# Kernel optimization log

Measured on AMD Instinct MI355X. Metric: run time of the kernel, lower is better.

Reference implementation:

```python
import jax, jax.numpy as jnp
import numpy as np

DIM = 512
HIDDEN = 2048
D_M = 256
R = 64
GEN_HIDDEN = D_M * 2  # hidden_mul=2
ALPHA_MEM = 1.0


def setup_inputs() -> dict:
    key = jax.random.key(0)
    ks = jax.random.split(key, 12)
    B, T = 2, 512
    inp = {
        'x': jax.random.normal(ks[0], (B, T, DIM), jnp.float32),
        'm_tok': jax.random.normal(ks[1], (B, T, D_M), jnp.float32),
        # base SwiGLU params
        'W1': jax.random.normal(ks[2], (HIDDEN, DIM), jnp.float32) * (1.0 / np.sqrt(DIM)),
        'W2': jax.random.normal(ks[3], (HIDDEN, DIM), jnp.float32) * (1.0 / np.sqrt(DIM)),
        'W3': jax.random.normal(ks[4], (DIM, HIDDEN), jnp.float32) * (1.0 / np.sqrt(HIDDEN)),
        'b1': jnp.zeros((HIDDEN,), jnp.float32),
        'b2': jnp.zeros((HIDDEN,), jnp.float32),
        'b3': jnp.zeros((DIM,), jnp.float32),
        # hypernetwork (FFNMemGenerator): d_m -> gen_hidden -> 3*r*dim
        'gen_w1': jax.random.normal(ks[5], (GEN_HIDDEN, D_M), jnp.float32) * (1.0 / np.sqrt(D_M)),
        'gen_b1': jnp.zeros((GEN_HIDDEN,), jnp.float32),
        'gen_w2': jax.random.normal(ks[6], (3 * R * DIM, GEN_HIDDEN), jnp.float32) * (0.02 / np.sqrt(GEN_HIDDEN)),
        'gen_b2': jnp.zeros((3 * R * DIM,), jnp.float32),
        'mem_gate': jnp.zeros((), jnp.float32),
    }
    return inp


def reference(x, m_tok, W1, W2, W3, b1, b2, b3, gen_w1, gen_b1, gen_w2, gen_b2, mem_gate):
    B, T, _ = x.shape
    # base SwiGLU FFN
    x1 = jnp.einsum('od,btd->bto', W1, x) + b1  # [B,T,hidden]
    x2 = jnp.einsum('od,btd->bto', W2, x) + b2
    h_base = jax.nn.silu(x1) * x2
    y_base = jnp.einsum('do,bto->btd', W3, h_base) + b3  # [B,T,dim]

    # hypernetwork-generated per-token low-rank weights
    hg = jax.nn.silu(jnp.einsum('hd,btd->bth', gen_w1, m_tok) + gen_b1)
    w = jnp.einsum('oh,bth->bto', gen_w2, hg) + gen_b2  # [B,T,3*r*dim]
    W1_m = w[..., : R * DIM].reshape(B, T, R, DIM)
    W2_m = w[..., R * DIM : 2 * R * DIM].reshape(B, T, R, DIM)
    W3_m = w[..., 2 * R * DIM :].reshape(B, T, DIM, R)

    # per-token batched matvecs (memory path)
    u1 = jnp.einsum('btrd,btd->btr', W1_m, x)
    u2 = jnp.einsum('btrd,btd->btr', W2_m, x)
    h_mem = jax.nn.silu(u1) * u2
    y_mem = jnp.einsum('btdr,btr->btd', W3_m, h_mem)

    g = jax.nn.sigmoid(mem_gate)
    return y_base + g * ALPHA_MEM * y_mem
```

## Files before the change

kernel.cpp:

```cpp
#include <hip/hip_runtime.h>
#include <cstdint>
#include <cstddef>

#define TOK   1024
#define DIMX  512
#define HID   2048
#define DM    256
#define GENH  512
#define RR    64
#define O3BASE 65536

typedef __bf16 bf16x8 __attribute__((ext_vector_type(8)));
typedef float  f32x4  __attribute__((ext_vector_type(4)));
typedef unsigned short u16x8 __attribute__((ext_vector_type(8)));

#define SB0 __builtin_amdgcn_sched_barrier(0)
#define BAR __builtin_amdgcn_s_barrier()

__device__ __forceinline__ unsigned short f2bf(float f) {
  union { float f; uint32_t u; } v; v.f = f;
  return (unsigned short)((v.u + 0x7fffu + ((v.u >> 16) & 1u)) >> 16);
}
__device__ __forceinline__ float bf2f(unsigned short h) {
  union { uint32_t u; float f; } v; v.u = (uint32_t)h << 16;
  return v.f;
}
__device__ __forceinline__ float silu_f(float x) { return x / (1.f + __expf(-x)); }

__device__ __forceinline__ u16x8 cvt8_hw(float4 a, float4 b) {
  union { __bf16 h; unsigned short u; } c;
  u16x8 r;
  c.h = (__bf16)a.x; r[0] = c.u; c.h = (__bf16)a.y; r[1] = c.u;
  c.h = (__bf16)a.z; r[2] = c.u; c.h = (__bf16)a.w; r[3] = c.u;
  c.h = (__bf16)b.x; r[4] = c.u; c.h = (__bf16)b.y; r[5] = c.u;
  c.h = (__bf16)b.z; r[6] = c.u; c.h = (__bf16)b.w; r[7] = c.u;
  return r;
}

__device__ __forceinline__ void async_copy16(const void* g, void* l) {
  __builtin_amdgcn_global_load_lds(
      (const __attribute__((address_space(1))) void*)g,
      (__attribute__((address_space(3))) void*)l, 16, 0, 0);
}

__device__ __forceinline__ float4 gldx4(const float* p) {
  float4 r;
  asm volatile("global_load_dwordx4 %0, %1, off" : "=v"(r) : "v"(p));
  return r;
}

__device__ __forceinline__ void cast8(const float* __restrict__ src,
                                      unsigned short* __restrict__ dst, size_t i) {
  float4 v0 = *(const float4*)(src + i);
  float4 v1 = *(const float4*)(src + i + 4);
  ushort4 h0, h1;
  h0.x = f2bf(v0.x); h0.y = f2bf(v0.y); h0.z = f2bf(v0.z); h0.w = f2bf(v0.w);
  h1.x = f2bf(v1.x); h1.y = f2bf(v1.y); h1.z = f2bf(v1.z); h1.w = f2bf(v1.w);
  *(ushort4*)(dst + i)     = h0;
  *(ushort4*)(dst + i + 4) = h1;
}

template<int ROWS>
__device__ __forceinline__ void stage_tile(
    const unsigned short* __restrict__ base, size_t row0, int stride, int kofs,
    unsigned short* Ls, int tid) {
  constexpr int IT = ROWS / 32;
  const int wave = tid >> 6, lane = tid & 63;
#pragma unroll
  for (int j = 0; j < IT; ++j) {
    int s   = wave * (IT * 64) + j * 64 + lane;
    int row = s >> 3;
    int kc  = (s & 7) ^ (row & 7);
    const unsigned short* g = base + (row0 + (size_t)row) * (size_t)stride + kofs + kc * 8;
    async_copy16(g, (char*)Ls + wave * (IT * 1024) + j * 1024);
  }
}

template<int KLEN, int MF>
__device__ __forceinline__ void mfma_tile_nt(
    const unsigned short* __restrict__ Abf, size_t a_row0, int astride,
    const unsigned short* __restrict__ Bbf, size_t b_row0, int bstride, int k0,
    unsigned short* As, unsigned short* Bs, f32x4 (&acc)[MF][4], int tid) {
  const int lane = tid & 63;
  const int wave = tid >> 6;
  const int m0 = (wave >> 1) * (MF * 16), n0 = (wave & 1) * 64;

  for (int kk = 0; kk < KLEN; kk += 64) {
    stage_tile<MF * 32>(Abf, a_row0, astride, k0 + kk, As, tid);
    stage_tile<128>(Bbf, b_row0, bstride, k0 + kk, Bs, tid);
    __syncthreads();
#pragma unroll
    for (int ks = 0; ks < 2; ++ks) {
      int cbase = ks * 4 + (lane >> 4);
      int koff  = (cbase ^ (lane & 7)) * 8;
      bf16x8 a[MF], b[4];
#pragma unroll
      for (int mf = 0; mf < MF; ++mf)
        a[mf] = *(const bf16x8*)(As + (m0 + mf * 16 + (lane & 15)) * 64 + koff);
#pragma unroll
      for (int nf = 0; nf < 4; ++nf)
        b[nf] = *(const bf16x8*)(Bs + (n0 + nf * 16 + (lane & 15)) * 64 + koff);
#pragma unroll
      for (int mf = 0; mf < MF; ++mf)
#pragma unroll
        for (int nf = 0; nf < 4; ++nf)
          acc[mf][nf] = __builtin_amdgcn_mfma_f32_16x16x32_bf16(
              a[mf], b[nf], acc[mf][nf], 0, 0, 0);
    }
    __syncthreads();
  }
}

template<int MF>
__device__ __forceinline__ void zero_accN(f32x4 (&acc)[MF][4]) {
#pragma unroll
  for (int i = 0; i < MF; ++i)
#pragma unroll
    for (int j = 0; j < 4; ++j) {
      f32x4 z = {0.f, 0.f, 0.f, 0.f};
      acc[i][j] = z;
    }
}

__device__ __forceinline__ void mfma_256_8ph(
    const unsigned short* __restrict__ Abf, size_t a_row0,
    const float* __restrict__ Bf, size_t b_row0,
    unsigned short* As, unsigned short* Bs, f32x4 (&acc)[8][4]) {
  const int tid = threadIdx.x, lane = tid & 63, wave = tid >> 6;
  const int wr = wave >> 2, wc = wave & 3;
  const int m0 = wr * 128, n0 = wc * 64;
  const int l15 = lane & 15;
  constexpr int ABUF = 256 * 64;
  constexpr int BBUF = 256 * 64;

  const float* gB[4];
  const unsigned short* gA[4];
  const int sbase = wave * 256 + lane;
#pragma unroll
  for (int jj = 0; jj < 4; ++jj) {
    int s = sbase + jj * 64;
    int row = s >> 3;
    int kc  = (s & 7) ^ (row & 7);
    gB[jj] = Bf + (b_row0 + (size_t)row) * GENH + kc * 8;
    gA[jj] = Abf + (a_row0 + (size_t)row) * GENH + kc * 8;
  }

  float4 v[8];
  bf16x8 bfr[4];
  bf16x8 afr[4];

  auto loadB = [&](int k0) {
#pragma unroll
    for (int jj = 0; jj < 4; ++jj) {
      v[2 * jj]     = gldx4(gB[jj] + k0);
      v[2 * jj + 1] = gldx4(gB[jj] + k0 + 4);
    }
  };
  auto stageA = [&](int k0, unsigned short* Ad) {
#pragma unroll
    for (int jj = 0; jj < 4; ++jj)
      async_copy16(gA[jj] + k0, (char*)Ad + (wave * 4 + jj) * 1024);
  };
  auto writeB = [&](unsigned short* Bd) {
#pragma unroll
    for (int jj = 0; jj < 4; ++jj) {
      int s = sbase + jj * 64;
      *(u16x8*)(Bd + s * 8) = cvt8_hw(v[2 * jj], v[2 * jj + 1]);
    }
  };
  auto rdB = [&](const unsigned short* Bb, int ks) {
    int koff = (((ks << 2) + (lane >> 4)) ^ (lane & 7)) << 3;
#pragma unroll
    for (int nf = 0; nf < 4; ++nf)
      bfr[nf] = *(const bf16x8*)(Bb + (n0 + nf * 16 + l15) * 64 + koff);
  };
  auto rdA = [&](const unsigned short* Ab, int ks, int mh) {
    int koff = (((ks << 2) + (lane >> 4)) ^ (lane & 7)) << 3;
#pragma unroll
    for (int i = 0; i < 4; ++i)
      afr[i] = *(const bf16x8*)(Ab + (m0 + (mh * 4 + i) * 16 + l15) * 64 + koff);
  };
  auto mfma16 = [&](int mh) {
    __builtin_amdgcn_s_setprio(1);
#pragma unroll
    for (int i = 0; i < 4; ++i)
#pragma unroll
      for (int nf = 0; nf < 4; ++nf)
        acc[mh * 4 + i][nf] = __builtin_amdgcn_mfma_f32_16x16x32_bf16(
            afr[i], bfr[nf], acc[mh * 4 + i][nf], 0, 0, 0);
    __builtin_amdgcn_s_setprio(0);
  };

  stageA(0, As);
  loadB(0);
  asm volatile("s_waitcnt vmcnt(0)" ::: "memory");
  SB0;
  writeB(Bs);
  __syncthreads();

  int cur = 0;
#pragma unroll 1
  for (int t = 0; t < 8; ++t) {
    unsigned short* Ac = As + cur * ABUF;
    unsigned short* Bc = Bs + cur * BBUF;
    unsigned short* An = As + (cur ^ 1) * ABUF;
    unsigned short* Bn = Bs + (cur ^ 1) * BBUF;
    const bool pf = (t < 7);
    const int k1 = (t + 1) * 64;

    rdB(Bc, 0); rdA(Ac, 0, 0);
    if (pf) loadB(k1);
    SB0; BAR; SB0;
    mfma16(0);
    SB0;
    rdA(Ac, 0, 1);
    mfma16(1);
    SB0; BAR;

    rdB(Bc, 1); rdA(Ac, 1, 0);
    if (pf) {
      stageA(k1, An);
      asm volatile("s_waitcnt vmcnt(4)" ::: "memory");
      SB0;
      writeB(Bn);
    }
    SB0; BAR; SB0;
    mfma16(0);
    SB0;
    rdA(Ac, 1, 1);
    mfma16(1);
    SB0;
    asm volatile("s_waitcnt vmcnt(0) lgkmcnt(0)" ::: "memory");
    BAR;
    cur ^= 1;
  }
}

__global__ __launch_bounds__(256) void prep_kernel(
    const float* __restrict__ x, const float* __restrict__ m_tok,
    const float* __restrict__ gen_w1, const float* __restrict__ gen_b1,
    const float* __restrict__ W1, const float* __restrict__ W2,
    const float* __restrict__ W3,
    unsigned short* __restrict__ xb, unsigned short* __restrict__ hgb,
    unsigned short* __restrict__ W1b, unsigned short* __restrict__ W2b,
    unsigned short* __restrict__ W3b) {
  __shared__ float mt[4 * DM];
  const int tid = threadIdx.x;
  const size_t t0 = (size_t)blockIdx.x * 4;
#pragma unroll
  for (int k = 0; k < 4; ++k) mt[k * 256 + tid] = m_tok[t0 * DM + k * 256 + tid];
#pragma unroll
  for (int k = 0; k < 8; ++k) {
    size_t idx = t0 * DIMX + k * 256 + tid;
    xb[idx] = f2bf(x[idx]);
  }
  {
    size_t base = ((size_t)blockIdx.x * 256 + tid) * 8;
#pragma unroll
    for (int it = 0; it < 2; ++it) {
      size_t idx = base + (size_t)it * 524288;
      cast8(W1, W1b, idx);
      cast8(W2, W2b, idx);
      cast8(W3, W3b, idx);
    }
  }
  __syncthreads();
#pragma unroll
  for (int hh = 0; hh < 2; ++hh) {
    int h = hh * 256 + tid;
    float a0, a1, a2, a3;
    a0 = a1 = a2 = a3 = gen_b1[h];
    const float* wr = gen_w1 + (size_t)h * DM;
    for (int d = 0; d < DM; d += 4) {
      float4 w = *(const float4*)(wr + d);
      a0 += w.x * mt[d]       + w.y * mt[d + 1]       + w.z * mt[d + 2]       + w.w * mt[d + 3];
      a1 += w.x * mt[256 + d] + w.y * mt[256 + d + 1] + w.z * mt[256 + d + 2] + w.w * mt[256 + d + 3];
      a2 += w.x * mt[512 + d] + w.y * mt[512 + d + 1] + w.z * mt[512 + d + 2] + w.w * mt[512 + d + 3];
      a3 += w.x * mt[768 + d] + w.y * mt[768 + d + 1] + w.z * mt[768 + d + 2] + w.w * mt[768 + d + 3];
    }
    hgb[(t0 + 0) * GENH + h] = f2bf(silu_f(a0));
    hgb[(t0 + 1) * GENH + h] = f2bf(silu_f(a1));
    hgb[(t0 + 2) * GENH + h] = f2bf(silu_f(a2));
    hgb[(t0 + 3) * GENH + h] = f2bf(silu_f(a3));
  }
}

__device__ __forceinline__ void ffn12_body(
    int bx, const unsigned short* __restrict__ xb, const unsigned short* __restrict__ W1b,
    const unsigned short* __restrict__ W2b, const float* __restrict__ pb1,
    const float* __restrict__ pb2, unsigned short* __restrict__ hb,
    unsigned short* As, unsigned short* B1s, unsigned short* B2s, int tid) {
  const int lane = tid & 63, wave = tid >> 6;
  const int ob = bx & 15, tb = bx >> 4;
  const size_t t0 = (size_t)tb * 32, o0 = (size_t)ob * 128;
  const int m0 = (wave >> 1) * 16, n0 = (wave & 1) * 64;

  f32x4 acc1[4], acc2[4];
#pragma unroll
  for (int j = 0; j < 4; ++j) {
    f32x4 z = {0.f, 0.f, 0.f, 0.f};
    acc1[j] = z; acc2[j] = z;
  }

  for (int kk = 0; kk < DIMX; kk += 64) {
    stage_tile<32>(xb, t0, DIMX, kk, As, tid);
    stage_tile<128>(W1b, o0, DIMX, kk, B1s, tid);
    stage_tile<128>(W2b, o0, DIMX, kk, B2s, tid);
    __syncthreads();
#pragma unroll
    for (int ks = 0; ks < 2; ++ks) {
      int cbase = ks * 4 + (lane >> 4);
      int koff  = (cbase ^ (lane & 7)) * 8;
      bf16x8 a, b1[4], b2[4];
      a = *(const bf16x8*)(As + (m0 + (lane & 15)) * 64 + koff);
#pragma unroll
      for (int nf = 0; nf < 4; ++nf) {
        b1[nf] = *(const bf16x8*)(B1s + (n0 + nf * 16 + (lane & 15)) * 64 + koff);
        b2[nf] = *(const bf16x8*)(B2s + (n0 + nf * 16 + (lane & 15)) * 64 + koff);
      }
#pragma unroll
      for (int nf = 0; nf < 4; ++nf) {
        acc1[nf] = __builtin_amdgcn_mfma_f32_16x16x32_bf16(a, b1[nf], acc1[nf], 0, 0, 0);
        acc2[nf] = __builtin_amdgcn_mfma_f32_16x16x32_bf16(a, b2[nf], acc2[nf], 0, 0, 0);
      }
    }
    __syncthreads();
  }

  const int q = lane >> 4;
  float b1v[4], b2v[4];
#pragma unroll
  for (int nf = 0; nf < 4; ++nf) {
    b1v[nf] = pb1[o0 + n0 + nf * 16 + (lane & 15)];
    b2v[nf] = pb2[o0 + n0 + nf * 16 + (lane & 15)];
  }
#pragma unroll
  for (int nf = 0; nf < 4; ++nf)
#pragma unroll
    for (int rg = 0; rg < 4; ++rg) {
      size_t trow = t0 + m0 + q * 4 + rg;
      size_t col  = o0 + n0 + nf * 16 + (lane & 15);
      float v1 = acc1[nf][rg] + b1v[nf];
      float v2 = acc2[nf][rg] + b2v[nf];
      hb[trow * HID + col] = f2bf(silu_f(v1) * v2);
    }
}

union SmemUV {
  struct { unsigned short As[2 * 256 * 64], Bs[2 * 256 * 64]; } ab;
  struct { unsigned short Xs[256 * 256]; } ep;
};

__device__ __forceinline__ void memuv_body(
    int bx, const unsigned short* __restrict__ hgb, const float* __restrict__ gw2,
    const float* __restrict__ gen_b2, const unsigned short* __restrict__ xb,
    float* __restrict__ up, SmemUV& sm) {
  const int s8 = bx & 7, w = bx >> 3;
  const int n = s8 * 32 + (w >> 2), m = w & 3;
  const size_t N0 = (size_t)n * 256, t0 = (size_t)m * 256;
  const int stripA = n << 1;
  const int j  = n >> 1;
  const int d0 = (stripA & 3) * 128;

  f32x4 acc[8][4];
  zero_accN<8>(acc);
  mfma_256_8ph(hgb, t0, gw2, N0, sm.ab.As, sm.ab.Bs, acc);

  const int tid = threadIdx.x, lane = tid & 63, wave = tid >> 6;
  const int wr = wave >> 2, wc = wave & 3;
#pragma unroll
  for (int i = 0; i < 16; ++i) {
    int qq = i * 512 + tid;
    int row = qq >> 5, c = qq & 31;
    const unsigned short* src = xb + (t0 + (size_t)row) * DIMX + d0 + c * 8;
    ushort4 v0 = *(const ushort4*)src;
    ushort4 v1 = *(const ushort4*)(src + 4);
    int cs = c ^ (((row >> 2) & 3) << 1);
    unsigned short* dst = sm.ep.Xs + row * 256 + cs * 8;
    *(ushort4*)dst = v0;
    *(ushort4*)(dst + 4) = v1;
  }
  __syncthreads();

  const int m0 = wr * 128, n0 = wc * 64;
  const int q = lane >> 4, l15 = lane & 15;
  float gbv[4];
#pragma unroll
  for (int i = 0; i < 4; ++i)
    gbv[i] = gen_b2[N0 + n0 + i * 16 + l15];

  const int p = ((stripA + (wc >> 1)) & 3) * 2 + (wc & 1);
  float* upd = up + (size_t)p * (128 * 1024) + (size_t)j * 1024 + t0;
#pragma unroll
  for (int mf = 0; mf < 8; ++mf) {
    f32x4 vals;
#pragma unroll
    for (int rg = 0; rg < 4; ++rg) {
      int trow = m0 + mf * 16 + q * 4 + rg;
      int swz  = ((trow >> 2) & 3) << 1;
      float val = 0.f;
#pragma unroll
      for (int nf = 0; nf < 4; ++nf) {
        int col = n0 + nf * 16 + l15;
        int gct = col >> 3;
        int idx = trow * 256 + ((gct ^ swz) << 3) + (col & 7);
        val += (acc[mf][nf][rg] + gbv[nf]) * bf2f(sm.ep.Xs[idx]);
      }
      val += __shfl_xor(val, 1);
      val += __shfl_xor(val, 2);
      val += __shfl_xor(val, 4);
      val += __shfl_xor(val, 8);
      vals[rg] = val;
    }
    if (l15 == 0)
      *(f32x4*)(upd + m0 + mf * 16 + q * 4) = vals;
  }
}

union SmemK2 {
  SmemUV m;
  struct { unsigned short As[2][32 * 64], B1s[2][128 * 64], B2s[2][128 * 64]; } f;
};

__global__ __launch_bounds__(512, 2) void k2_kernel(
    const unsigned short* __restrict__ xb, const unsigned short* __restrict__ W1b,
    const unsigned short* __restrict__ W2b, const float* __restrict__ b1,
    const float* __restrict__ b2, unsigned short* __restrict__ hb,
    const unsigned short* __restrict__ hgb, const float* __restrict__ gw2,
    const float* __restrict__ gen_b2, float* __restrict__ up) {
  __shared__ SmemK2 sm;
  const int bx = blockIdx.x;
  if (bx < 1024) {
    memuv_body(bx, hgb, gw2, gen_b2, xb, up, sm.m);
  } else {
    const int sub = threadIdx.x >> 8, tloc = threadIdx.x & 255;
    const int vb = (bx - 1024) * 2 + sub;
    ffn12_body(vb, xb, W1b, W2b, b1, b2, hb,
               sm.f.As[sub], sm.f.B1s[sub], sm.f.B2s[sub], tloc);
  }
}

__device__ __forceinline__ void gemm3p_body(
    int bx, const unsigned short* __restrict__ hb, const unsigned short* __restrict__ W3b,
    float* __restrict__ yp, unsigned short* As, unsigned short* Bs) {
  const int slice = bx >> 6, r6 = bx & 63;
  const int ob = r6 & 3, tb = r6 >> 2;
  const size_t o0 = (size_t)ob * 128, t0 = (size_t)tb * 64;
  const int k0 = slice * 512;
  const int tid = threadIdx.x;
  f32x4 acc[2][4];
  zero_accN<2>(acc);
  mfma_tile_nt<512, 2>(hb, t0, HID, W3b, o0, HID, k0, As, Bs, acc, tid);

  const int lane = tid & 63, wave = tid >> 6;
  const int m0 = (wave >> 1) * 32, n0 = (wave & 1) * 64;
  float* out = yp + (size_t)slice * (TOK * DIMX);
#pragma unroll
  for (int nf = 0; nf < 4; ++nf) {
    int nn = n0 + nf * 16 + (lane & 15);
#pragma unroll
    for (int mf = 0; mf < 2; ++mf) {
      int mb = m0 + mf * 16 + ((lane >> 4) << 2);
#pragma unroll
      for (int rg = 0; rg < 4; ++rg)
        out[(t0 + mb + rg) * DIMX + o0 + nn] = acc[mf][nf][rg];
    }
  }
}

__device__ __forceinline__ void hmem_body(int bx, const float* __restrict__ up,
                                          float* __restrict__ hm) {
  int i = bx * 256 + threadIdx.x;
  int t = i & 1023, r = i >> 10;
  float u1 = 0.f, u2 = 0.f;
#pragma unroll
  for (int p = 0; p < 8; ++p) {
    u1 += up[(size_t)p * (128 * 1024) + (size_t)r * 1024 + t];
    u2 += up[(size_t)p * (128 * 1024) + (size_t)(64 + r) * 1024 + t];
  }
  hm[(size_t)t * RR + r] = silu_f(u1) * u2;
}

union SmemK3 {
  struct { unsigned short As[64 * 64], Bs[128 * 64]; } g;
};

__global__ __launch_bounds__(256) void k3_kernel(
    const unsigned short* __restrict__ hb, const unsigned short* __restrict__ W3b,
    float* __restrict__ yp, const float* __restrict__ up, float* __restrict__ hm) {
  __shared__ SmemK3 sm;
  const int bx = blockIdx.x;
  if (bx < 256)
    gemm3p_body(bx, hb, W3b, yp, sm.g.As, sm.g.Bs);
  else
    hmem_body(bx - 256, up, hm);
}

union SmemY {
  struct { unsigned short As[2 * 256 * 64], Bs[2 * 256 * 64]; } ab;
  struct { float Hs[256 * 64]; } ep;
};

__global__ __launch_bounds__(512, 2) void memy_kernel(
    const unsigned short* __restrict__ hgb, const float* __restrict__ gw2,
    const float* __restrict__ gen_b2, const float* __restrict__ hmem,
    const float* __restrict__ yp, const float* __restrict__ b3,
    const float* __restrict__ mem_gate, float* __restrict__ y) {
  __shared__ SmemY sm;
  const int bx = blockIdx.x;
  const int s8 = bx & 7, w = bx >> 3;
  const int n = s8 * 16 + (w >> 2), m = w & 3;
  const size_t N0 = (size_t)n * 256;
  const size_t brow0 = (size_t)O3BASE + N0;
  const size_t t0 = (size_t)m * 256;

  f32x4 acc[8][4];
  zero_accN<8>(acc);
  mfma_256_8ph(hgb, t0, gw2, brow0, sm.ab.As, sm.ab.Bs, acc);

  const int tid = threadIdx.x, lane = tid & 63, wave = tid >> 6;
  const int wr = wave >> 2, wc = wave & 3;
#pragma unroll
  for (int i = 0; i < 8; ++i) {
    int qq = i * 512 + tid;
    int row = qq >> 4, c = qq & 15;
    float4 vv = *(const float4*)(hmem + (t0 + (size_t)row) * RR + c * 4);
    int cs = c ^ (((row >> 2) & 3) << 2);
    *(float4*)(sm.ep.Hs + row * 64 + cs * 4) = vv;
  }
  __syncthreads();

  const int m0 = wr * 128, n0 = wc * 64;
  const int q = lane >> 4, l15 = lane & 15;
  const float g = 1.f / (1.f + __expf(-mem_gate[0]));
  float gbv[4];
#pragma unroll
  for (int i = 0; i < 4; ++i)
    gbv[i] = gen_b2[brow0 + n0 + i * 16 + l15];

  const int d = (int)(N0 >> 6) + wc;
  const float b3v = b3[d];
#pragma unroll
  for (int mf = 0; mf < 8; ++mf)
#pragma unroll
    for (int rg = 0; rg < 4; ++rg) {
      int trow = m0 + mf * 16 + q * 4 + rg;
      int swz  = ((trow >> 2) & 3) << 2;
      float val = 0.f;
#pragma unroll
      for (int nf = 0; nf < 4; ++nf) {
        int r = nf * 16 + l15;
        int idx = trow * 64 + (((r >> 2) ^ swz) << 2) + (r & 3);
        val += (acc[mf][nf][rg] + gbv[nf]) * sm.ep.Hs[idx];
      }
      val += __shfl_xor(val, 1);
      val += __shfl_xor(val, 2);
      val += __shfl_xor(val, 4);
      val += __shfl_xor(val, 8);
      if (l15 == 0) {
        size_t gi = (t0 + trow) * DIMX + d;
        float base = b3v + yp[gi]
                   + yp[(size_t)1 * (TOK * DIMX) + gi]
                   + yp[(size_t)2 * (TOK * DIMX) + gi]
                   + yp[(size_t)3 * (TOK * DIMX) + gi];
        y[gi] = base + g * val;
      }
    }
}

extern "C" void kernel_launch(void* const* d_in, const int* in_sizes, int n_in,
                              void* d_out, int out_size, void* d_ws, size_t ws_size,
                              hipStream_t stream) {
  const float* x        = (const float*)d_in[0];
  const float* m_tok    = (const float*)d_in[1];
  const float* W1       = (const float*)d_in[2];
  const float* W2       = (const float*)d_in[3];
  const float* W3       = (const float*)d_in[4];
  const float* b1       = (const float*)d_in[5];
  const float* b2       = (const float*)d_in[6];
  const float* b3       = (const float*)d_in[7];
  const float* gen_w1   = (const float*)d_in[8];
  const float* gen_b1   = (const float*)d_in[9];
  const float* gen_w2   = (const float*)d_in[10];
  const float* gen_b2   = (const float*)d_in[11];
  const float* mem_gate = (const float*)d_in[12];
  float* y = (float*)d_out;

  char* ws = (char*)d_ws;
#define KB(v) ((size_t)(v) << 10)
  unsigned short* xb  = (unsigned short*)(ws);
  unsigned short* hgb = (unsigned short*)(ws + KB(1024));
  unsigned short* hb  = (unsigned short*)(ws + KB(2048));
  float* up  = (float*)(ws + KB(6144));
  float* hm  = (float*)(ws + KB(10240));
  float* yp  = (float*)(ws + KB(10752));
  unsigned short* W1b = (unsigned short*)(ws + KB(21248));
  unsigned short* W2b = (unsigned short*)(ws + KB(23296));
  unsigned short* W3b = (unsigned short*)(ws + KB(25344));
#undef KB

  prep_kernel<<<256, 256, 0, stream>>>(x, m_tok, gen_w1, gen_b1, W1, W2, W3,
                                       xb, hgb, W1b, W2b, W3b);
  k2_kernel<<<1024 + 256, 512, 0, stream>>>(xb, W1b, W2b, b1, b2, hb,
                                            hgb, gen_w2, gen_b2, up);
  k3_kernel<<<256 + 256, 256, 0, stream>>>(hb, W3b, yp, up, hm);
  memy_kernel<<<512, 512, 0, stream>>>(hgb, gen_w2, gen_b2, hm, yp, b3,
                                       mem_gate, y);
}
```

Baseline: 476.2 us.

## Pre-cast gen_w2 to bf16 and stage both GEMM operands via async LDS copies

gen_w2 is now converted to bf16 in a separate workspace buffer. The first two-thirds are cast by extra blocks in prep_kernel, and the W3_m slice is cast by extra blocks in k2_kernel that run alongside the memuv GEMM. The shared 256x256 GEMM mainloop then loads both A and B with global_load_lds async copies instead of fp32 register loads plus conversion and LDS writes, which simplifies the barrier schedule. The cost is an extra full read and write of the 100MB fp32 weight each call. The fp32-to-bf16 conversion is now done in software rounding rather than hardware cvt.

```diff
diff --git a/kernel.cpp b/kernel.cpp
--- a/kernel.cpp
+++ b/kernel.cpp
@@ -12,10 +12,8 @@
 
 typedef __bf16 bf16x8 __attribute__((ext_vector_type(8)));
 typedef float  f32x4  __attribute__((ext_vector_type(4)));
-typedef unsigned short u16x8 __attribute__((ext_vector_type(8)));
 
 #define SB0 __builtin_amdgcn_sched_barrier(0)
-#define BAR __builtin_amdgcn_s_barrier()
 
 __device__ __forceinline__ unsigned short f2bf(float f) {
   union { float f; uint32_t u; } v; v.f = f;
@@ -26,27 +24,11 @@
   return v.f;
 }
 __device__ __forceinline__ float silu_f(float x) { return x / (1.f + __expf(-x)); }
-
-__device__ __forceinline__ u16x8 cvt8_hw(float4 a, float4 b) {
-  union { __bf16 h; unsigned short u; } c;
-  u16x8 r;
-  c.h = (__bf16)a.x; r[0] = c.u; c.h = (__bf16)a.y; r[1] = c.u;
-  c.h = (__bf16)a.z; r[2] = c.u; c.h = (__bf16)a.w; r[3] = c.u;
-  c.h = (__bf16)b.x; r[4] = c.u; c.h = (__bf16)b.y; r[5] = c.u;
-  c.h = (__bf16)b.z; r[6] = c.u; c.h = (__bf16)b.w; r[7] = c.u;
-  return r;
-}
 
 __device__ __forceinline__ void async_copy16(const void* g, void* l) {
   __builtin_amdgcn_global_load_lds(
       (const __attribute__((address_space(1))) void*)g,
       (__attribute__((address_space(3))) void*)l, 16, 0, 0);
-}
-
-__device__ __forceinline__ float4 gldx4(const float* p) {
-  float4 r;
-  asm volatile("global_load_dwordx4 %0, %1, off" : "=v"(r) : "v"(p));
-  return r;
 }
 
 __device__ __forceinline__ void cast8(const float* __restrict__ src,
@@ -122,51 +104,36 @@
     }
 }
 
-__device__ __forceinline__ void mfma_256_8ph(
+__device__ __forceinline__ void mfma_256_async(
     const unsigned short* __restrict__ Abf, size_t a_row0,
-    const float* __restrict__ Bf, size_t b_row0,
+    const unsigned short* __restrict__ Bbf, size_t b_row0,
     unsigned short* As, unsigned short* Bs, f32x4 (&acc)[8][4]) {
   const int tid = threadIdx.x, lane = tid & 63, wave = tid >> 6;
   const int wr = wave >> 2, wc = wave & 3;
   const int m0 = wr * 128, n0 = wc * 64;
   const int l15 = lane & 15;
-  constexpr int ABUF = 256 * 64;
-  constexpr int BBUF = 256 * 64;
-
-  const float* gB[4];
-  const unsigned short* gA[4];
+  constexpr int ABUF = 256 * 64, BBUF = 256 * 64;
+
+  const unsigned short *gA[4], *gB[4];
   const int sbase = wave * 256 + lane;
 #pragma unroll
   for (int jj = 0; jj < 4; ++jj) {
     int s = sbase + jj * 64;
     int row = s >> 3;
     int kc  = (s & 7) ^ (row & 7);
-    gB[jj] = Bf + (b_row0 + (size_t)row) * GENH + kc * 8;
     gA[jj] = Abf + (a_row0 + (size_t)row) * GENH + kc * 8;
-  }
-
-  float4 v[8];
-  bf16x8 bfr[4];
-  bf16x8 afr[4];
-
-  auto loadB = [&](int k0) {
-#pragma unroll
-    for (int jj = 0; jj < 4; ++jj) {
-      v[2 * jj]     = gldx4(gB[jj] + k0);
-      v[2 * jj + 1] = gldx4(gB[jj] + k0 + 4);
-    }
-  };
-  auto stageA = [&](int k0, unsigned short* Ad) {
+    gB[jj] = Bbf + (b_row0 + (size_t)row) * GENH + kc * 8;
+  }
+
+  bf16x8 bfr[4], afr[4];
+
+  auto stage = [&](int k0, unsigned short* Ad, unsigned short* Bd) {
 #pragma unroll
     for (int jj = 0; jj < 4; ++jj)
       async_copy16(gA[jj] + k0, (char*)Ad + (wave * 4 + jj) * 1024);
-  };
-  auto writeB = [&](unsigned short* Bd) {
-#pragma unroll
-    for (int jj = 0; jj < 4; ++jj) {
-      int s = sbase + jj * 64;
-      *(u16x8*)(Bd + s * 8) = cvt8_hw(v[2 * jj], v[2 * jj + 1]);
-    }
+#pragma unroll
+    for (int jj = 0; jj < 4; ++jj)
+      async_copy16(gB[jj] + k0, (char*)Bd + (wave * 4 + jj) * 1024);
   };
   auto rdB = [&](const unsigned short* Bb, int ks) {
     int koff = (((ks << 2) + (lane >> 4)) ^ (lane & 7)) << 3;
@@ -191,11 +158,8 @@
     __builtin_amdgcn_s_setprio(0);
   };
 
-  stageA(0, As);
-  loadB(0);
+  stage(0, As, Bs);
   asm volatile("s_waitcnt vmcnt(0)" ::: "memory");
-  SB0;
-  writeB(Bs);
   __syncthreads();
 
   int cur = 0;
@@ -203,35 +167,23 @@
   for (int t = 0; t < 8; ++t) {
     unsigned short* Ac = As + cur * ABUF;
     unsigned short* Bc = Bs + cur * BBUF;
-    unsigned short* An = As + (cur ^ 1) * ABUF;
-    unsigned short* Bn = Bs + (cur ^ 1) * BBUF;
-    const bool pf = (t < 7);
-    const int k1 = (t + 1) * 64;
-
+    if (t < 7)
+      stage((t + 1) * 64, As + (cur ^ 1) * ABUF, Bs + (cur ^ 1) * BBUF);
+    SB0;
     rdB(Bc, 0); rdA(Ac, 0, 0);
-    if (pf) loadB(k1);
-    SB0; BAR; SB0;
     mfma16(0);
     SB0;
     rdA(Ac, 0, 1);
     mfma16(1);
-    SB0; BAR;
-
+    SB0;
     rdB(Bc, 1); rdA(Ac, 1, 0);
-    if (pf) {
-      stageA(k1, An);
-      asm volatile("s_waitcnt vmcnt(4)" ::: "memory");
-      SB0;
-      writeB(Bn);
-    }
-    SB0; BAR; SB0;
     mfma16(0);
     SB0;
     rdA(Ac, 1, 1);
     mfma16(1);
     SB0;
-    asm volatile("s_waitcnt vmcnt(0) lgkmcnt(0)" ::: "memory");
-    BAR;
+    asm volatile("s_waitcnt vmcnt(0)" ::: "memory");
+    __syncthreads();
     cur ^= 1;
   }
 }
@@ -240,12 +192,21 @@
     const float* __restrict__ x, const float* __restrict__ m_tok,
     const float* __restrict__ gen_w1, const float* __restrict__ gen_b1,
     const float* __restrict__ W1, const float* __restrict__ W2,
-    const float* __restrict__ W3,
+    const float* __restrict__ W3, const float* __restrict__ gen_w2,
     unsigned short* __restrict__ xb, unsigned short* __restrict__ hgb,
     unsigned short* __restrict__ W1b, unsigned short* __restrict__ W2b,
-    unsigned short* __restrict__ W3b) {
+    unsigned short* __restrict__ W3b, unsigned short* __restrict__ w2b) {
+  const int tid = threadIdx.x;
+  if (blockIdx.x >= 256) {
+    const size_t cb = blockIdx.x - 256;
+#pragma unroll
+    for (int k = 0; k < 8; ++k) {
+      size_t i = ((size_t)k * 524288 + cb * 256 + tid) * 8;
+      cast8(gen_w2, w2b, i);
+    }
+    return;
+  }
   __shared__ float mt[4 * DM];
-  const int tid = threadIdx.x;
   const size_t t0 = (size_t)blockIdx.x * 4;
 #pragma unroll
   for (int k = 0; k < 4; ++k) mt[k * 256 + tid] = m_tok[t0 * DM + k * 256 + tid];
@@ -352,7 +313,7 @@
 };
 
 __device__ __forceinline__ void memuv_body(
-    int bx, const unsigned short* __restrict__ hgb, const float* __restrict__ gw2,
+    int bx, const unsigned short* __restrict__ hgb, const unsigned short* __restrict__ w2b,
     const float* __restrict__ gen_b2, const unsigned short* __restrict__ xb,
     float* __restrict__ up, SmemUV& sm) {
   const int s8 = bx & 7, w = bx >> 3;
@@ -364,7 +325,7 @@
 
   f32x4 acc[8][4];
   zero_accN<8>(acc);
-  mfma_256_8ph(hgb, t0, gw2, N0, sm.ab.As, sm.ab.Bs, acc);
+  mfma_256_async(hgb, t0, w2b, N0, sm.ab.As, sm.ab.Bs, acc);
 
   const int tid = threadIdx.x, lane = tid & 63, wave = tid >> 6;
   const int wr = wave >> 2, wc = wave & 3;
@@ -427,16 +388,24 @@
     const unsigned short* __restrict__ W2b, const float* __restrict__ b1,
     const float* __restrict__ b2, unsigned short* __restrict__ hb,
     const unsigned short* __restrict__ hgb, const float* __restrict__ gw2,
-    const float* __restrict__ gen_b2, float* __restrict__ up) {
+    unsigned short* __restrict__ w2b, const float* __restrict__ gen_b2,
+    float* __restrict__ up) {
   __shared__ SmemK2 sm;
   const int bx = blockIdx.x;
   if (bx < 1024) {
-    memuv_body(bx, hgb, gw2, gen_b2, xb, up, sm.m);
-  } else {
+    memuv_body(bx, hgb, w2b, gen_b2, xb, up, sm.m);
+  } else if (bx < 1280) {
     const int sub = threadIdx.x >> 8, tloc = threadIdx.x & 255;
     const int vb = (bx - 1024) * 2 + sub;
     ffn12_body(vb, xb, W1b, W2b, b1, b2, hb,
                sm.f.As[sub], sm.f.B1s[sub], sm.f.B2s[sub], tloc);
+  } else {
+    const size_t cb = bx - 1280, tid = threadIdx.x;
+#pragma unroll
+    for (int k = 0; k < 16; ++k) {
+      size_t i = 33554432 + ((size_t)k * 131072 + cb * 512 + tid) * 8;
+      cast8(gw2, w2b, i);
+    }
   }
 }
 
@@ -502,7 +471,7 @@
 };
 
 __global__ __launch_bounds__(512, 2) void memy_kernel(
-    const unsigned short* __restrict__ hgb, const float* __restrict__ gw2,
+    const unsigned short* __restrict__ hgb, const unsigned short* __restrict__ w2b,
     const float* __restrict__ gen_b2, const float* __restrict__ hmem,
     const float* __restrict__ yp, const float* __restrict__ b3,
     const float* __restrict__ mem_gate, float* __restrict__ y) {
@@ -516,7 +485,7 @@
 
   f32x4 acc[8][4];
   zero_accN<8>(acc);
-  mfma_256_8ph(hgb, t0, gw2, brow0, sm.ab.As, sm.ab.Bs, acc);
+  mfma_256_async(hgb, t0, w2b, brow0, sm.ab.As, sm.ab.Bs, acc);
 
   const int tid = threadIdx.x, lane = tid & 63, wave = tid >> 6;
   const int wr = wave >> 2, wc = wave & 3;
@@ -597,13 +566,15 @@
   unsigned short* W1b = (unsigned short*)(ws + KB(21248));
   unsigned short* W2b = (unsigned short*)(ws + KB(23296));
   unsigned short* W3b = (unsigned short*)(ws + KB(25344));
+  unsigned short* w2b = (unsigned short*)(ws + KB(27392));
 #undef KB
 
-  prep_kernel<<<256, 256, 0, stream>>>(x, m_tok, gen_w1, gen_b1, W1, W2, W3,
-                                       xb, hgb, W1b, W2b, W3b);
-  k2_kernel<<<1024 + 256, 512, 0, stream>>>(xb, W1b, W2b, b1, b2, hb,
-                                            hgb, gen_w2, gen_b2, up);
+  prep_kernel<<<256 + 2048, 256, 0, stream>>>(x, m_tok, gen_w1, gen_b1,
+                                              W1, W2, W3, gen_w2,
+                                              xb, hgb, W1b, W2b, W3b, w2b);
+  k2_kernel<<<1024 + 256 + 256, 512, 0, stream>>>(xb, W1b, W2b, b1, b2, hb,
+                                                  hgb, gen_w2, w2b, gen_b2, up);
   k3_kernel<<<256 + 256, 256, 0, stream>>>(hb, W3b, yp, up, hm);
-  memy_kernel<<<512, 512, 0, stream>>>(hgb, gen_w2, gen_b2, hm, yp, b3,
+  memy_kernel<<<512, 512, 0, stream>>>(hgb, w2b, gen_b2, hm, yp, b3,
                                        mem_gate, y);
 }
```

Measured after the change: 479.8 us. Within noise of the previous version (+0.8%).
